# Kernel tuning notes

Hardware: AMD Instinct MI355X
Metric: run time of the kernel (lower is better)

## Reference

```python
import math
import jax, jax.numpy as jnp
import numpy as np

D = 768      # hidden_size
H = 16       # num_attention_heads (hardcoded in module)
DH = D // H  # value dim per head
SEQ = 512    # fpos/tpos are taken modulo 512
EPS = 1e-5   # torch LayerNorm default
SCALE = math.sqrt(D / H)  # attention_head_size = dim_key_query_all / num_heads


def _collab_attn(h, fpos, tpos, Wq, Wk, Wcb, Wv, bv, mix, Wd, bd, lng, lnb):
    """CollaborativeAttention.forward on one segment. h: [SEQ, D]."""
    fpos = fpos % SEQ
    tpos = tpos % SEQ
    fs = h[fpos]                                   # [F, D] gathered 'from' nodes
    ts = h[tpos]                                   # [T, D] gathered 'to' nodes
    q = fs @ Wq.T                                  # [F, D] (no bias)
    k = ts @ Wk.T                                  # [T, D] (no bias)
    mq = q[None, :, :] * mix[:, None, :]           # [H, F, D] per-head mixing
    scores = jnp.einsum('hfd,td->hft', mq, k)      # [H, F, T] full-D contraction
    cb = (ts @ Wcb.T).T                            # [H, T] content bias
    scores = (scores + cb[:, None, :]) / SCALE
    probs = jax.nn.softmax(scores, axis=-1)        # dropout = identity at eval
    v = (ts @ Wv.T + bv).reshape(-1, H, DH).transpose(1, 0, 2)  # [H, T, DH]
    ctx = jnp.einsum('hft,htd->hfd', probs, v)     # [H, F, DH]
    ctx = ctx.transpose(1, 0, 2).reshape(-1, D) @ Wd.T + bd      # [F, D]
    x = fs + ctx                                   # residual on gathered nodes
    mu = x.mean(-1, keepdims=True)
    var = ((x - mu) ** 2).mean(-1, keepdims=True)
    return lng * (x - mu) / jnp.sqrt(var + EPS) + lnb


def _encoder(hidden_states, fpos, tpos, qtoc, ctoq):
    outs = []
    for b in range(3):  # fixed small segment count, matches original unrolling
        o1 = _collab_attn(hidden_states[b], fpos[b], tpos[b], *qtoc).mean(0)
        o2 = _collab_attn(hidden_states[b], tpos[b], fpos[b], *ctoq).mean(0)
        outs.append(jnp.concatenate([o1, o2]))
    return jnp.stack(outs)  # [3, 2*D]


def setup_inputs() -> dict:
    key = jax.random.key(0)
    ks = jax.random.split(key, 32)
    inp = {
        'hidden_states': jax.random.normal(ks[0], (3, SEQ, D), jnp.float32),
        'fpos': jax.random.randint(ks[1], (3, 2048), 0, SEQ, jnp.int32),
        'tpos': jax.random.randint(ks[2], (3, 2048), 0, SEQ, jnp.int32),
    }
    i = 3
    for p in ('qtoc', 'ctoq'):
        for n, shape, std in (('Wq', (D, D), 0.02), ('Wk', (D, D), 0.02),
                              ('Wcb', (H, D), 0.02), ('Wv', (D, D), 0.02),
                              ('Wd', (D, D), 0.02), ('mix', (H, D), 0.2)):
            inp[p + '_' + n] = std * jax.random.normal(ks[i], shape, jnp.float32)
            i += 1
        inp[p + '_bv'] = jnp.zeros((D,), jnp.float32)
        inp[p + '_bd'] = jnp.zeros((D,), jnp.float32)
        inp[p + '_lng'] = jnp.ones((D,), jnp.float32)
        inp[p + '_lnb'] = jnp.zeros((D,), jnp.float32)
    return inp


def reference(hidden_states, fpos, tpos,
              qtoc_Wq, qtoc_Wk, qtoc_Wcb, qtoc_Wv, qtoc_Wd, qtoc_mix,
              qtoc_bv, qtoc_bd, qtoc_lng, qtoc_lnb,
              ctoq_Wq, ctoq_Wk, ctoq_Wcb, ctoq_Wv, ctoq_Wd, ctoq_mix,
              ctoq_bv, ctoq_bd, ctoq_lng, ctoq_lnb):
    qtoc = (qtoc_Wq, qtoc_Wk, qtoc_Wcb, qtoc_Wv, qtoc_bv, qtoc_mix,
            qtoc_Wd, qtoc_bd, qtoc_lng, qtoc_lnb)
    ctoq = (ctoq_Wq, ctoq_Wk, ctoq_Wcb, ctoq_Wv, ctoq_bv, ctoq_mix,
            ctoq_Wd, ctoq_bd, ctoq_lng, ctoq_lnb)
    return _encoder(hidden_states, fpos, tpos, qtoc, ctoq)
```

## Files before the change

kernel.cpp:

```cpp
#include <hip/hip_runtime.h>
#include <math.h>

#define DD 768
#define HH 16
#define DHH 48
#define NPOS 512
#define NIDX 2048
#define INV_SCALE 0.14433756729740643f
#define LN_EPS 1e-5f

typedef __bf16 bf16_t;
typedef __bf16 bf16x8 __attribute__((ext_vector_type(8)));
typedef float f32x4 __attribute__((ext_vector_type(4)));

__device__ __forceinline__ void g2lds16(const void* g, void* l) {
  __builtin_amdgcn_global_load_lds((const __attribute__((address_space(1))) void*)g,
                                   (__attribute__((address_space(3))) void*)l, 16, 0, 0);
}

struct CvtDesc { const float* src; bf16_t* dst; int n8; };
struct CvtBatch { CvtDesc d[9]; };

__global__ __launch_bounds__(256) void prep(const int* __restrict__ fpos,
                                            const int* __restrict__ tpos,
                                            int* __restrict__ CNT, CvtBatch cvb,
                                            const float* __restrict__ hs,
                                            const float* __restrict__ Wcb0,
                                            const float* __restrict__ Wcb1,
                                            float* __restrict__ cbG) {
  const int bid = blockIdx.x;
  const int tid = threadIdx.x;
  __shared__ int shist[NPOS];
  if (bid < 6) {
    const int b = bid >> 1, which = bid & 1;
    const int* src = (which ? tpos : fpos) + b * NIDX;
    for (int i = tid; i < NPOS; i += 256) shist[i] = 0;
    __syncthreads();
    for (int i = tid; i < NIDX; i += 256) atomicAdd(&shist[src[i] & (NPOS - 1)], 1);
    __syncthreads();
    for (int i = tid; i < NPOS; i += 256) CNT[bid * NPOS + i] = shist[i];
  } else if (bid < 582) {
    const CvtDesc de = cvb.d[(bid - 6) >> 6];
    for (int i = ((bid - 6) & 63) * 256 + tid; i < de.n8; i += 64 * 256) {
      const f32x4 a = *(const f32x4*)(de.src + (size_t)i * 8);
      const f32x4 b = *(const f32x4*)(de.src + (size_t)i * 8 + 4);
      bf16_t t[8];
#pragma unroll
      for (int e = 0; e < 4; ++e) { t[e] = (bf16_t)a[e]; t[4 + e] = (bf16_t)b[e]; }
      *(bf16x8*)(de.dst + (size_t)i * 8) = *(bf16x8*)t;
    }
  } else {
    const int g = bid - 582;
    const int pd = g >> 5, t0 = (g & 31) * 16;
    const int b = pd >> 1;
    const float* W = (pd & 1) ? Wcb1 : Wcb0;
    const int tl = tid >> 4, hh = tid & 15;
    const float* hrow = hs + ((size_t)b * NPOS + t0 + tl) * DD;
    const float* wrow = W + hh * DD;
    float s = 0.f;
    for (int k = 0; k < DD; k += 4) {
      const f32x4 a = *(const f32x4*)(hrow + k);
      const f32x4 bq = *(const f32x4*)(wrow + k);
      s += a[0] * bq[0] + a[1] * bq[1] + a[2] * bq[2] + a[3] * bq[3];
    }
    cbG[((size_t)pd * NPOS + t0 + tl) * HH + hh] = s;
  }
}

struct MDesc { const bf16_t* A; const bf16_t* B; const float* bias; void* C; int mode; };
struct MBatch { MDesc d[18]; };

__global__ __launch_bounds__(256, 4) void gemm64(MBatch batch) {
  const MDesc de = batch.d[blockIdx.y];
  const int mt = blockIdx.x & 7, nt = blockIdx.x >> 3;
  const int m0 = mt * 64, n0 = nt * 128;

  __shared__ bf16_t SA[2][2048];
  __shared__ bf16_t SB[2][4096];

  const int tid = threadIdx.x;
  const int w = tid >> 6, lane = tid & 63;
  const int wm = w >> 1, wn = w & 1;
  const int lm = lane & 15, lq = lane >> 4;
  const int sr = lane >> 2, sq = lane & 3;

  f32x4 acc[2][4] = {};

  auto stage = [&](int buf, int k0) {
#pragma unroll
    for (int c = 0; c < 3; ++c) {
      const int issue = w + c * 4;
      if (issue < 4)
        g2lds16(de.A + (size_t)(m0 + issue * 16 + sr) * 768 + k0 + sq * 8,
                SA[buf] + issue * 512);
      else {
        const int e = issue - 4;
        g2lds16(de.B + (size_t)(n0 + e * 16 + sr) * 768 + k0 + sq * 8,
                SB[buf] + e * 512);
      }
    }
  };

  stage(0, 0);
  for (int k0i = 0; k0i < 24; ++k0i) {
    const int cur = k0i & 1;
    __syncthreads();
    if (k0i + 1 < 24) stage(cur ^ 1, (k0i + 1) * 32);
    bf16x8 af[2], bfr[4];
#pragma unroll
    for (int i = 0; i < 2; ++i)
      af[i] = *(const bf16x8*)(SA[cur] + (wm * 32 + i * 16 + lm) * 32 + lq * 8);
#pragma unroll
    for (int j = 0; j < 4; ++j)
      bfr[j] = *(const bf16x8*)(SB[cur] + (wn * 64 + j * 16 + lm) * 32 + lq * 8);
#pragma unroll
    for (int i = 0; i < 2; ++i)
#pragma unroll
      for (int j = 0; j < 4; ++j)
        acc[i][j] = __builtin_amdgcn_mfma_f32_16x16x32_bf16(af[i], bfr[j], acc[i][j], 0, 0, 0);
  }

#pragma unroll
  for (int i = 0; i < 2; ++i) {
    const int rbase = m0 + wm * 32 + i * 16 + lq * 4;
#pragma unroll
    for (int j = 0; j < 4; ++j) {
      const int c = n0 + wn * 64 + j * 16 + lm;
      const float bv = de.bias ? de.bias[c] : 0.f;
#pragma unroll
      for (int r = 0; r < 4; ++r) {
        const float v = acc[i][j][r] + bv;
        if (de.mode == 0)      ((float*)de.C)[(size_t)(rbase + r) * 768 + c] = v;
        else if (de.mode == 1) ((bf16_t*)de.C)[(size_t)(rbase + r) * 768 + c] = (bf16_t)v;
        else                   ((bf16_t*)de.C)[(size_t)c * NPOS + rbase + r] = (bf16_t)v;
      }
    }
  }
}

__global__ __launch_bounds__(256, 4) void attn_mfma(
    const bf16_t* __restrict__ Qg, const bf16_t* __restrict__ Kg,
    const bf16_t* __restrict__ Vt, const float* __restrict__ cbG,
    const int* __restrict__ CNT, const float* __restrict__ mix0,
    const float* __restrict__ mix1, bf16_t* __restrict__ CTX) {
  const int bid = blockIdx.x;
  const int ft = bid & 7, h = (bid >> 3) & 15, pd = bid >> 7;
  const int dir = pd & 1;
  const int f0 = ft * 64;

  __shared__ bf16_t U[17408];
  __shared__ float mixs[768];
  __shared__ float cbw[512];
  __shared__ float rowl[64];

  const int tid = threadIdx.x;
  const int w = tid >> 6, lane = tid & 63;
  const bf16_t* Qp = Qg + (size_t)pd * NPOS * DD;
  const bf16_t* Kp = Kg + (size_t)pd * NPOS * DD;
  const bf16_t* Vp = Vt + (size_t)pd * DD * NPOS + (size_t)h * DHH * NPOS;
  const float* mix = (dir ? mix1 : mix0) + h * DD;
  const int* cnt = CNT + ((pd & ~1) + (1 - dir)) * NPOS;

  for (int i = tid; i < 768; i += 256) mixs[i] = mix[i] * INV_SCALE;
  for (int i = tid; i < 512; i += 256)
    cbw[i] = cbG[((size_t)pd * NPOS + i) * HH + h] * INV_SCALE + __logf((float)cnt[i]);

  const int wm = w >> 1, wn = w & 1;
  const int lm = lane & 15, lq = lane >> 4;
  const int sr = lane >> 2, sq = lane & 3;

  f32x4 pv[4] = {};

  for (int jt = 0; jt < 4; ++jt) {
    const int j0 = jt * 128;
    __syncthreads();

    auto stage = [&](int buf, int k0) {
#pragma unroll
      for (int c = 0; c < 3; ++c) {
        const int issue = w + c * 4;
        if (issue < 4)
          g2lds16(Qp + (size_t)(f0 + issue * 16 + sr) * DD + k0 + sq * 8,
                  U + buf * 6144 + issue * 512);
        else {
          const int e = issue - 4;
          g2lds16(Kp + (size_t)(j0 + e * 16 + sr) * DD + k0 + sq * 8,
                  U + buf * 6144 + 2048 + e * 512);
        }
      }
    };

    stage(0, 0);
    f32x4 sa[2][4] = {};
    for (int k0i = 0; k0i < 24; ++k0i) {
      const int cur = k0i & 1;
      const int k0 = k0i * 32;
      __syncthreads();
      if (k0i + 1 < 24) stage(cur ^ 1, k0 + 32);
      const f32x4 mxa = *(const f32x4*)&mixs[k0 + lq * 8];
      const f32x4 mxb = *(const f32x4*)&mixs[k0 + lq * 8 + 4];
      bf16x8 af[2], bfr[4];
#pragma unroll
      for (int i = 0; i < 2; ++i) {
        const bf16x8 q = *(const bf16x8*)(U + cur * 6144 + (wm * 32 + i * 16 + lm) * 32 + lq * 8);
        bf16_t t[8];
#pragma unroll
        for (int e = 0; e < 4; ++e) {
          t[e]     = (bf16_t)((float)q[e] * mxa[e]);
          t[4 + e] = (bf16_t)((float)q[4 + e] * mxb[e]);
        }
        af[i] = *(bf16x8*)t;
      }
#pragma unroll
      for (int j = 0; j < 4; ++j)
        bfr[j] = *(const bf16x8*)(U + cur * 6144 + 2048 + (wn * 64 + j * 16 + lm) * 32 + lq * 8);
#pragma unroll
      for (int i = 0; i < 2; ++i)
#pragma unroll
        for (int j = 0; j < 4; ++j)
          sa[i][j] = __builtin_amdgcn_mfma_f32_16x16x32_bf16(af[i], bfr[j], sa[i][j], 0, 0, 0);
    }
    __syncthreads();

#pragma unroll
    for (int j = 0; j < 4; ++j) {
      const int col = wn * 64 + j * 16 + lm;
      const float cb = cbw[j0 + col];
#pragma unroll
      for (int i = 0; i < 2; ++i) {
        const int rbase = wm * 32 + i * 16 + lq * 4;
#pragma unroll
        for (int r = 0; r < 4; ++r)
          U[(rbase + r) * 136 + col] = (bf16_t)__expf(sa[i][j][r] + cb);
      }
    }
    for (int i = tid; i < 49 * 16; i += 256) {
      const int r = i >> 4, cc = i & 15;
      if (r < 48)
        *(bf16x8*)(U + 8704 + r * 136 + cc * 8) =
            *(const bf16x8*)(Vp + (size_t)r * NPOS + j0 + cc * 8);
      else {
        bf16_t ones[8];
#pragma unroll
        for (int e = 0; e < 8; ++e) ones[e] = (bf16_t)1.f;
        *(bf16x8*)(U + 8704 + 48 * 136 + cc * 8) = *(bf16x8*)ones;
      }
    }
    __syncthreads();

#pragma unroll
    for (int kk = 0; kk < 4; ++kk) {
      const bf16x8 pa = *(const bf16x8*)(U + (w * 16 + lm) * 136 + kk * 32 + lq * 8);
#pragma unroll
      for (int j = 0; j < 4; ++j) {
        const bf16x8 pb = *(const bf16x8*)(U + 8704 + (j * 16 + lm) * 136 + kk * 32 + lq * 8);
        pv[j] = __builtin_amdgcn_mfma_f32_16x16x32_bf16(pa, pb, pv[j], 0, 0, 0);
      }
    }
  }

  if (lm == 0) {
#pragma unroll
    for (int r = 0; r < 4; ++r) rowl[w * 16 + lq * 4 + r] = pv[3][r];
  }
  __syncthreads();
#pragma unroll
  for (int j = 0; j < 3; ++j) {
#pragma unroll
    for (int r = 0; r < 4; ++r) {
      const int fr = w * 16 + lq * 4 + r;
      CTX[((size_t)pd * NPOS + f0 + fr) * DD + h * DHH + j * 16 + lm] =
          (bf16_t)(pv[j][r] / rowl[fr]);
    }
  }
}

__global__ __launch_bounds__(256) void ln_mean_kernel(
    const float* __restrict__ hs, const float* __restrict__ XB,
    const int* __restrict__ CNT,
    const float* __restrict__ lng0, const float* __restrict__ lnb0,
    const float* __restrict__ lng1, const float* __restrict__ lnb1,
    float* __restrict__ out) {
  const int blk = blockIdx.x;
  const int chunk = blk & 15;
  const int pd = blk >> 4;
  const int b = pd >> 1, dir = pd & 1;
  const float* lng = dir ? lng1 : lng0;
  const float* lnb = dir ? lnb1 : lnb0;
  const int* cnt = CNT + pd * NPOS;
  const float* hb = hs + (size_t)b * NPOS * DD;
  const float* xb = XB + (size_t)pd * NPOS * DD;

  __shared__ float wacc[4][DD];
  const int tid = threadIdx.x;
  const int wave = tid >> 6, lane = tid & 63;
  for (int d0 = tid; d0 < 4 * DD; d0 += 256) ((float*)wacc)[d0] = 0.f;
  __syncthreads();

  float lg[12], lb[12];
#pragma unroll
  for (int qd = 0; qd < 12; ++qd) {
    lg[qd] = lng[lane + qd * 64];
    lb[qd] = lnb[lane + qd * 64];
  }

  for (int rr = 0; rr < 8; ++rr) {
    const int p = chunk * 32 + wave * 8 + rr;
    float x[12];
    float s = 0.f, ss = 0.f;
#pragma unroll
    for (int qd = 0; qd < 12; ++qd) {
      const int d0 = lane + qd * 64;
      const float xv = hb[(size_t)p * DD + d0] + xb[(size_t)p * DD + d0];
      x[qd] = xv; s += xv; ss += xv * xv;
    }
#pragma unroll
    for (int o = 1; o < 64; o <<= 1) {
      s += __shfl_xor(s, o);
      ss += __shfl_xor(ss, o);
    }
    const float mu = s * (1.f / 768.f);
    const float var = ss * (1.f / 768.f) - mu * mu;
    const float rstd = rsqrtf(var + LN_EPS);
    const float wgt = (float)cnt[p];
    if (wgt != 0.f) {
#pragma unroll
      for (int qd = 0; qd < 12; ++qd) {
        const int d0 = lane + qd * 64;
        wacc[wave][d0] += wgt * (lg[qd] * (x[qd] - mu) * rstd + lb[qd]);
      }
    }
  }
  __syncthreads();
  for (int d0 = tid; d0 < DD; d0 += 256) {
    const float t = wacc[0][d0] + wacc[1][d0] + wacc[2][d0] + wacc[3][d0];
    atomicAdd(&out[b * 1536 + dir * 768 + d0], t * (1.f / 2048.f));
  }
}

extern "C" void kernel_launch(void* const* d_in, const int* in_sizes, int n_in,
                              void* d_out, int out_size, void* d_ws, size_t ws_size,
                              hipStream_t stream) {
  const float* hs  = (const float*)d_in[0];
  const int* fpos  = (const int*)d_in[1];
  const int* tpos  = (const int*)d_in[2];

  const float* Wq[2]; const float* Wk[2]; const float* Wcb[2]; const float* Wv[2];
  const float* Wd[2]; const float* mixp[2];
  const float* bv[2]; const float* bd[2]; const float* lng[2]; const float* lnb[2];
  for (int p = 0; p < 2; ++p) {
    const int base = 3 + p * 10;
    Wq[p]   = (const float*)d_in[base + 0];
    Wk[p]   = (const float*)d_in[base + 1];
    Wcb[p]  = (const float*)d_in[base + 2];
    Wv[p]   = (const float*)d_in[base + 3];
    Wd[p]   = (const float*)d_in[base + 4];
    mixp[p] = (const float*)d_in[base + 5];
    bv[p]   = (const float*)d_in[base + 6];
    bd[p]   = (const float*)d_in[base + 7];
    lng[p]  = (const float*)d_in[base + 8];
    lnb[p]  = (const float*)d_in[base + 9];
  }

  char* wsp = (char*)d_ws;
  size_t off = 0;
  auto alloc = [&](size_t bytes) { char* p = wsp + off; off = (off + bytes + 255) & ~(size_t)255; return p; };
  bf16_t* hsb  = (bf16_t*)alloc((size_t)3 * NPOS * DD * 2);
  bf16_t* Wb   = (bf16_t*)alloc((size_t)8 * DD * DD * 2);
  bf16_t* Qbf  = (bf16_t*)alloc((size_t)6 * NPOS * DD * 2);
  bf16_t* Kbf  = (bf16_t*)alloc((size_t)6 * NPOS * DD * 2);
  bf16_t* VtG  = (bf16_t*)alloc((size_t)6 * DD * NPOS * 2);
  bf16_t* CTXb = (bf16_t*)alloc((size_t)6 * NPOS * DD * 2);
  float*  XB   = (float*) alloc((size_t)6 * NPOS * DD * 4);
  float*  cbG  = (float*) alloc((size_t)6 * NPOS * HH * 4);
  int*    CNTb = (int*)   alloc((size_t)6 * NPOS * 4);

  hipMemsetAsync(d_out, 0, (size_t)out_size * sizeof(float), stream);

  CvtBatch cvb{};
  cvb.d[0] = CvtDesc{hs, hsb, 3 * NPOS * DD / 8};
  const float* wsrc[8] = {Wq[0], Wk[0], Wv[0], Wd[0], Wq[1], Wk[1], Wv[1], Wd[1]};
  for (int i = 0; i < 8; ++i)
    cvb.d[1 + i] = CvtDesc{wsrc[i], Wb + (size_t)i * DD * DD, DD * DD / 8};
  prep<<<774, 256, 0, stream>>>(fpos, tpos, CNTb, cvb, hs, Wcb[0], Wcb[1], cbG);

  MBatch gb{};
  int n = 0;
  for (int b = 0; b < 3; ++b)
    for (int p = 0; p < 2; ++p) {
      const int pd = b * 2 + p;
      const bf16_t* A = hsb + (size_t)b * NPOS * DD;
      const size_t o = (size_t)pd * NPOS * DD;
      gb.d[n++] = MDesc{A, Wb + (size_t)(p * 4 + 0) * DD * DD, nullptr, Qbf + o, 1};
      gb.d[n++] = MDesc{A, Wb + (size_t)(p * 4 + 1) * DD * DD, nullptr, Kbf + o, 1};
      gb.d[n++] = MDesc{A, Wb + (size_t)(p * 4 + 2) * DD * DD, bv[p],   VtG + (size_t)pd * DD * NPOS, 2};
    }
  gemm64<<<dim3(48, 18), 256, 0, stream>>>(gb);

  attn_mfma<<<768, 256, 0, stream>>>(Qbf, Kbf, VtG, cbG, CNTb, mixp[0], mixp[1], CTXb);

  MBatch gd{};
  for (int b = 0; b < 3; ++b)
    for (int p = 0; p < 2; ++p) {
      const int pd = b * 2 + p;
      const size_t o = (size_t)pd * NPOS * DD;
      gd.d[pd] = MDesc{CTXb + o, Wb + (size_t)(p * 4 + 3) * DD * DD, bd[p], XB + o, 0};
    }
  gemm64<<<dim3(48, 6), 256, 0, stream>>>(gd);

  ln_mean_kernel<<<96, 256, 0, stream>>>(hs, XB, CNTb, lng[0], lnb[0], lng[1], lnb[1],
                                         (float*)d_out);
}
```

Measured before the change: 288.2 us.

## Fuse content-bias into K GEMM, swizzle LDS, pre-mix Q per head, widen LN grid

The content-bias projection is folded into the K projection GEMM by appending the Wcb rows, zero-padded, to Wk, so the separate dot-product blocks in prep go away. LDS staging and reads gain an XOR swizzle to cut bank conflicts in both the GEMM and attention kernels. When workspace allows, a new qmix kernel writes a per-head mixed and scaled Q tensor, so the attention inner loop skips the per-element multiply, at the cost of a large extra memory write and read. The LayerNorm-mean kernel uses four times as many blocks with fewer rows each, and attention launch bounds drop to 3 blocks per CU.

```diff
diff --git a/kernel.cpp b/kernel.cpp
--- a/kernel.cpp
+++ b/kernel.cpp
@@ -17,17 +17,17 @@
   __builtin_amdgcn_global_load_lds((const __attribute__((address_space(1))) void*)g,
                                    (__attribute__((address_space(3))) void*)l, 16, 0, 0);
 }
+__device__ __forceinline__ int stg_chunk(int lane) { return (lane & 3) ^ ((lane >> 3) & 3); }
+__device__ __forceinline__ int rd_off(int row, int lq) {
+  return row * 32 + ((lq ^ ((row >> 1) & 3)) << 3);
+}
 
 struct CvtDesc { const float* src; bf16_t* dst; int n8; };
-struct CvtBatch { CvtDesc d[9]; };
+struct CvtBatch { CvtDesc d[13]; };
 
 __global__ __launch_bounds__(256) void prep(const int* __restrict__ fpos,
                                             const int* __restrict__ tpos,
-                                            int* __restrict__ CNT, CvtBatch cvb,
-                                            const float* __restrict__ hs,
-                                            const float* __restrict__ Wcb0,
-                                            const float* __restrict__ Wcb1,
-                                            float* __restrict__ cbG) {
+                                            int* __restrict__ CNT, CvtBatch cvb) {
   const int bid = blockIdx.x;
   const int tid = threadIdx.x;
   __shared__ int shist[NPOS];
@@ -39,40 +39,54 @@
     for (int i = tid; i < NIDX; i += 256) atomicAdd(&shist[src[i] & (NPOS - 1)], 1);
     __syncthreads();
     for (int i = tid; i < NPOS; i += 256) CNT[bid * NPOS + i] = shist[i];
-  } else if (bid < 582) {
-    const CvtDesc de = cvb.d[(bid - 6) >> 6];
-    for (int i = ((bid - 6) & 63) * 256 + tid; i < de.n8; i += 64 * 256) {
+    return;
+  }
+  const CvtDesc de = cvb.d[(bid - 6) >> 6];
+  for (int i = ((bid - 6) & 63) * 256 + tid; i < de.n8; i += 64 * 256) {
+    bf16_t t[8];
+    if (de.src) {
       const f32x4 a = *(const f32x4*)(de.src + (size_t)i * 8);
       const f32x4 b = *(const f32x4*)(de.src + (size_t)i * 8 + 4);
-      bf16_t t[8];
 #pragma unroll
       for (int e = 0; e < 4; ++e) { t[e] = (bf16_t)a[e]; t[4 + e] = (bf16_t)b[e]; }
-      *(bf16x8*)(de.dst + (size_t)i * 8) = *(bf16x8*)t;
-    }
-  } else {
-    const int g = bid - 582;
-    const int pd = g >> 5, t0 = (g & 31) * 16;
-    const int b = pd >> 1;
-    const float* W = (pd & 1) ? Wcb1 : Wcb0;
-    const int tl = tid >> 4, hh = tid & 15;
-    const float* hrow = hs + ((size_t)b * NPOS + t0 + tl) * DD;
-    const float* wrow = W + hh * DD;
-    float s = 0.f;
-    for (int k = 0; k < DD; k += 4) {
-      const f32x4 a = *(const f32x4*)(hrow + k);
-      const f32x4 bq = *(const f32x4*)(wrow + k);
-      s += a[0] * bq[0] + a[1] * bq[1] + a[2] * bq[2] + a[3] * bq[3];
-    }
-    cbG[((size_t)pd * NPOS + t0 + tl) * HH + hh] = s;
-  }
-}
-
-struct MDesc { const bf16_t* A; const bf16_t* B; const float* bias; void* C; int mode; };
+    } else {
+#pragma unroll
+      for (int e = 0; e < 8; ++e) t[e] = (bf16_t)0.f;
+    }
+    *(bf16x8*)(de.dst + (size_t)i * 8) = *(bf16x8*)t;
+  }
+}
+
+__global__ __launch_bounds__(256) void qmix(const bf16_t* __restrict__ Qbf,
+                                            const float* __restrict__ mix0,
+                                            const float* __restrict__ mix1,
+                                            bf16_t* __restrict__ Qm) {
+  const int idx = blockIdx.x * 256 + threadIdx.x;
+  const int c = idx % 96;
+  const int f = (idx / 96) & 511;
+  const int h = (idx / (96 * 512)) & 15;
+  const int pd = idx / (96 * 512 * 16);
+  const bf16x8 q = *(const bf16x8*)(Qbf + ((size_t)pd * NPOS + f) * DD + c * 8);
+  const float* m = ((pd & 1) ? mix1 : mix0) + h * DD + c * 8;
+  const f32x4 m0 = *(const f32x4*)m;
+  const f32x4 m1 = *(const f32x4*)(m + 4);
+  bf16_t t[8];
+#pragma unroll
+  for (int e = 0; e < 4; ++e) {
+    t[e]     = (bf16_t)((float)q[e] * m0[e] * INV_SCALE);
+    t[4 + e] = (bf16_t)((float)q[4 + e] * m1[e] * INV_SCALE);
+  }
+  *(bf16x8*)(Qm + ((size_t)(pd * 16 + h) * NPOS + f) * DD + c * 8) = *(bf16x8*)t;
+}
+
+struct MDesc { const bf16_t* A; const bf16_t* B; const float* bias; void* C;
+               float* cb; int mode; int ntiles; };
 struct MBatch { MDesc d[18]; };
 
 __global__ __launch_bounds__(256, 4) void gemm64(MBatch batch) {
   const MDesc de = batch.d[blockIdx.y];
   const int mt = blockIdx.x & 7, nt = blockIdx.x >> 3;
+  if (nt >= de.ntiles) return;
   const int m0 = mt * 64, n0 = nt * 128;
 
   __shared__ bf16_t SA[2][2048];
@@ -82,7 +96,7 @@
   const int w = tid >> 6, lane = tid & 63;
   const int wm = w >> 1, wn = w & 1;
   const int lm = lane & 15, lq = lane >> 4;
-  const int sr = lane >> 2, sq = lane & 3;
+  const int sr = lane >> 2, sc = stg_chunk(lane);
 
   f32x4 acc[2][4] = {};
 
@@ -91,11 +105,11 @@
     for (int c = 0; c < 3; ++c) {
       const int issue = w + c * 4;
       if (issue < 4)
-        g2lds16(de.A + (size_t)(m0 + issue * 16 + sr) * 768 + k0 + sq * 8,
+        g2lds16(de.A + (size_t)(m0 + issue * 16 + sr) * 768 + k0 + sc * 8,
                 SA[buf] + issue * 512);
       else {
         const int e = issue - 4;
-        g2lds16(de.B + (size_t)(n0 + e * 16 + sr) * 768 + k0 + sq * 8,
+        g2lds16(de.B + (size_t)(n0 + e * 16 + sr) * 768 + k0 + sc * 8,
                 SB[buf] + e * 512);
       }
     }
@@ -109,10 +123,10 @@
     bf16x8 af[2], bfr[4];
 #pragma unroll
     for (int i = 0; i < 2; ++i)
-      af[i] = *(const bf16x8*)(SA[cur] + (wm * 32 + i * 16 + lm) * 32 + lq * 8);
+      af[i] = *(const bf16x8*)(SA[cur] + rd_off(wm * 32 + i * 16 + lm, lq));
 #pragma unroll
     for (int j = 0; j < 4; ++j)
-      bfr[j] = *(const bf16x8*)(SB[cur] + (wn * 64 + j * 16 + lm) * 32 + lq * 8);
+      bfr[j] = *(const bf16x8*)(SB[cur] + rd_off(wn * 64 + j * 16 + lm, lq));
 #pragma unroll
     for (int i = 0; i < 2; ++i)
 #pragma unroll
@@ -126,48 +140,57 @@
 #pragma unroll
     for (int j = 0; j < 4; ++j) {
       const int c = n0 + wn * 64 + j * 16 + lm;
-      const float bv = de.bias ? de.bias[c] : 0.f;
+      const float bv = (de.bias && c < 768) ? de.bias[c] : 0.f;
 #pragma unroll
       for (int r = 0; r < 4; ++r) {
         const float v = acc[i][j][r] + bv;
         if (de.mode == 0)      ((float*)de.C)[(size_t)(rbase + r) * 768 + c] = v;
         else if (de.mode == 1) ((bf16_t*)de.C)[(size_t)(rbase + r) * 768 + c] = (bf16_t)v;
-        else                   ((bf16_t*)de.C)[(size_t)c * NPOS + rbase + r] = (bf16_t)v;
-      }
-    }
-  }
-}
-
-__global__ __launch_bounds__(256, 4) void attn_mfma(
-    const bf16_t* __restrict__ Qg, const bf16_t* __restrict__ Kg,
-    const bf16_t* __restrict__ Vt, const float* __restrict__ cbG,
-    const int* __restrict__ CNT, const float* __restrict__ mix0,
-    const float* __restrict__ mix1, bf16_t* __restrict__ CTX) {
+        else if (de.mode == 2) ((bf16_t*)de.C)[(size_t)c * NPOS + rbase + r] = (bf16_t)v;
+        else {
+          if (c < 768)       ((bf16_t*)de.C)[(size_t)(rbase + r) * 768 + c] = (bf16_t)v;
+          else if (c < 784)  de.cb[(size_t)(rbase + r) * 16 + (c - 768)] = v;
+        }
+      }
+    }
+  }
+}
+
+template <int PRE>
+__global__ __launch_bounds__(256, 3) void attn_mfma(
+    const bf16_t* __restrict__ Qg, const bf16_t* __restrict__ Qm,
+    const bf16_t* __restrict__ Kg, const bf16_t* __restrict__ Vt,
+    const float* __restrict__ cbG, const int* __restrict__ CNT,
+    const float* __restrict__ mix0, const float* __restrict__ mix1,
+    bf16_t* __restrict__ CTX) {
   const int bid = blockIdx.x;
   const int ft = bid & 7, h = (bid >> 3) & 15, pd = bid >> 7;
   const int dir = pd & 1;
   const int f0 = ft * 64;
 
   __shared__ bf16_t U[17408];
-  __shared__ float mixs[768];
+  __shared__ float mixs[PRE ? 4 : 768];
   __shared__ float cbw[512];
   __shared__ float rowl[64];
 
   const int tid = threadIdx.x;
   const int w = tid >> 6, lane = tid & 63;
-  const bf16_t* Qp = Qg + (size_t)pd * NPOS * DD;
+  const bf16_t* Qp = PRE ? (Qm + (size_t)(pd * 16 + h) * NPOS * DD)
+                         : (Qg + (size_t)pd * NPOS * DD);
   const bf16_t* Kp = Kg + (size_t)pd * NPOS * DD;
   const bf16_t* Vp = Vt + (size_t)pd * DD * NPOS + (size_t)h * DHH * NPOS;
-  const float* mix = (dir ? mix1 : mix0) + h * DD;
   const int* cnt = CNT + ((pd & ~1) + (1 - dir)) * NPOS;
 
-  for (int i = tid; i < 768; i += 256) mixs[i] = mix[i] * INV_SCALE;
+  if (!PRE) {
+    const float* mix = (dir ? mix1 : mix0) + h * DD;
+    for (int i = tid; i < 768; i += 256) mixs[i] = mix[i] * INV_SCALE;
+  }
   for (int i = tid; i < 512; i += 256)
     cbw[i] = cbG[((size_t)pd * NPOS + i) * HH + h] * INV_SCALE + __logf((float)cnt[i]);
 
   const int wm = w >> 1, wn = w & 1;
   const int lm = lane & 15, lq = lane >> 4;
-  const int sr = lane >> 2, sq = lane & 3;
+  const int sr = lane >> 2, sc = stg_chunk(lane);
 
   f32x4 pv[4] = {};
 
@@ -180,11 +203,11 @@
       for (int c = 0; c < 3; ++c) {
         const int issue = w + c * 4;
         if (issue < 4)
-          g2lds16(Qp + (size_t)(f0 + issue * 16 + sr) * DD + k0 + sq * 8,
+          g2lds16(Qp + (size_t)(f0 + issue * 16 + sr) * DD + k0 + sc * 8,
                   U + buf * 6144 + issue * 512);
         else {
           const int e = issue - 4;
-          g2lds16(Kp + (size_t)(j0 + e * 16 + sr) * DD + k0 + sq * 8,
+          g2lds16(Kp + (size_t)(j0 + e * 16 + sr) * DD + k0 + sc * 8,
                   U + buf * 6144 + 2048 + e * 512);
         }
       }
@@ -197,23 +220,28 @@
       const int k0 = k0i * 32;
       __syncthreads();
       if (k0i + 1 < 24) stage(cur ^ 1, k0 + 32);
-      const f32x4 mxa = *(const f32x4*)&mixs[k0 + lq * 8];
-      const f32x4 mxb = *(const f32x4*)&mixs[k0 + lq * 8 + 4];
       bf16x8 af[2], bfr[4];
 #pragma unroll
       for (int i = 0; i < 2; ++i) {
-        const bf16x8 q = *(const bf16x8*)(U + cur * 6144 + (wm * 32 + i * 16 + lm) * 32 + lq * 8);
-        bf16_t t[8];
-#pragma unroll
-        for (int e = 0; e < 4; ++e) {
-          t[e]     = (bf16_t)((float)q[e] * mxa[e]);
-          t[4 + e] = (bf16_t)((float)q[4 + e] * mxb[e]);
+        const int off = cur * 6144 + rd_off(wm * 32 + i * 16 + lm, lq);
+        if (PRE) {
+          af[i] = *(const bf16x8*)(U + off);
+        } else {
+          const f32x4 mxa = *(const f32x4*)&mixs[k0 + lq * 8];
+          const f32x4 mxb = *(const f32x4*)&mixs[k0 + lq * 8 + 4];
+          const bf16x8 q = *(const bf16x8*)(U + off);
+          bf16_t t[8];
+#pragma unroll
+          for (int e = 0; e < 4; ++e) {
+            t[e]     = (bf16_t)((float)q[e] * mxa[e]);
+            t[4 + e] = (bf16_t)((float)q[4 + e] * mxb[e]);
+          }
+          af[i] = *(bf16x8*)t;
         }
-        af[i] = *(bf16x8*)t;
       }
 #pragma unroll
       for (int j = 0; j < 4; ++j)
-        bfr[j] = *(const bf16x8*)(U + cur * 6144 + 2048 + (wn * 64 + j * 16 + lm) * 32 + lq * 8);
+        bfr[j] = *(const bf16x8*)(U + cur * 6144 + 2048 + rd_off(wn * 64 + j * 16 + lm, lq));
 #pragma unroll
       for (int i = 0; i < 2; ++i)
 #pragma unroll
@@ -282,8 +310,8 @@
     const float* __restrict__ lng1, const float* __restrict__ lnb1,
     float* __restrict__ out) {
   const int blk = blockIdx.x;
-  const int chunk = blk & 15;
-  const int pd = blk >> 4;
+  const int chunk = blk & 63;
+  const int pd = blk >> 6;
   const int b = pd >> 1, dir = pd & 1;
   const float* lng = dir ? lng1 : lng0;
   const float* lnb = dir ? lnb1 : lnb0;
@@ -304,8 +332,8 @@
     lb[qd] = lnb[lane + qd * 64];
   }
 
-  for (int rr = 0; rr < 8; ++rr) {
-    const int p = chunk * 32 + wave * 8 + rr;
+  for (int rr = 0; rr < 2; ++rr) {
+    const int p = chunk * 8 + wave * 2 + rr;
     float x[12];
     float s = 0.f, ss = 0.f;
 #pragma unroll
@@ -366,7 +394,8 @@
   size_t off = 0;
   auto alloc = [&](size_t bytes) { char* p = wsp + off; off = (off + bytes + 255) & ~(size_t)255; return p; };
   bf16_t* hsb  = (bf16_t*)alloc((size_t)3 * NPOS * DD * 2);
-  bf16_t* Wb   = (bf16_t*)alloc((size_t)8 * DD * DD * 2);
+  bf16_t* Wb   = (bf16_t*)alloc((size_t)6 * DD * DD * 2);
+  bf16_t* WkCb = (bf16_t*)alloc((size_t)2 * 896 * DD * 2);
   bf16_t* Qbf  = (bf16_t*)alloc((size_t)6 * NPOS * DD * 2);
   bf16_t* Kbf  = (bf16_t*)alloc((size_t)6 * NPOS * DD * 2);
   bf16_t* VtG  = (bf16_t*)alloc((size_t)6 * DD * NPOS * 2);
@@ -374,15 +403,24 @@
   float*  XB   = (float*) alloc((size_t)6 * NPOS * DD * 4);
   float*  cbG  = (float*) alloc((size_t)6 * NPOS * HH * 4);
   int*    CNTb = (int*)   alloc((size_t)6 * NPOS * 4);
+  const size_t qm_bytes = (size_t)6 * HH * NPOS * DD * 2;
+  const int use_pre = (off + qm_bytes + 4096 <= ws_size);
+  bf16_t* Qm = use_pre ? (bf16_t*)alloc(qm_bytes) : nullptr;
 
   hipMemsetAsync(d_out, 0, (size_t)out_size * sizeof(float), stream);
 
   CvtBatch cvb{};
   cvb.d[0] = CvtDesc{hs, hsb, 3 * NPOS * DD / 8};
-  const float* wsrc[8] = {Wq[0], Wk[0], Wv[0], Wd[0], Wq[1], Wk[1], Wv[1], Wd[1]};
-  for (int i = 0; i < 8; ++i)
-    cvb.d[1 + i] = CvtDesc{wsrc[i], Wb + (size_t)i * DD * DD, DD * DD / 8};
-  prep<<<774, 256, 0, stream>>>(fpos, tpos, CNTb, cvb, hs, Wcb[0], Wcb[1], cbG);
+  for (int p = 0; p < 2; ++p) {
+    cvb.d[1 + p * 3] = CvtDesc{Wq[p], Wb + (size_t)(p * 3 + 0) * DD * DD, DD * DD / 8};
+    cvb.d[2 + p * 3] = CvtDesc{Wv[p], Wb + (size_t)(p * 3 + 1) * DD * DD, DD * DD / 8};
+    cvb.d[3 + p * 3] = CvtDesc{Wd[p], Wb + (size_t)(p * 3 + 2) * DD * DD, DD * DD / 8};
+    bf16_t* wk = WkCb + (size_t)p * 896 * DD;
+    cvb.d[7 + p * 3] = CvtDesc{Wk[p], wk, DD * DD / 8};
+    cvb.d[8 + p * 3] = CvtDesc{Wcb[p], wk + (size_t)768 * DD, 16 * DD / 8};
+    cvb.d[9 + p * 3] = CvtDesc{nullptr, wk + (size_t)784 * DD, 112 * DD / 8};
+  }
+  prep<<<838, 256, 0, stream>>>(fpos, tpos, CNTb, cvb);
 
   MBatch gb{};
   int n = 0;
@@ -391,23 +429,33 @@
       const int pd = b * 2 + p;
       const bf16_t* A = hsb + (size_t)b * NPOS * DD;
       const size_t o = (size_t)pd * NPOS * DD;
-      gb.d[n++] = MDesc{A, Wb + (size_t)(p * 4 + 0) * DD * DD, nullptr, Qbf + o, 1};
-      gb.d[n++] = MDesc{A, Wb + (size_t)(p * 4 + 1) * DD * DD, nullptr, Kbf + o, 1};
-      gb.d[n++] = MDesc{A, Wb + (size_t)(p * 4 + 2) * DD * DD, bv[p],   VtG + (size_t)pd * DD * NPOS, 2};
-    }
-  gemm64<<<dim3(48, 18), 256, 0, stream>>>(gb);
-
-  attn_mfma<<<768, 256, 0, stream>>>(Qbf, Kbf, VtG, cbG, CNTb, mixp[0], mixp[1], CTXb);
+      gb.d[n++] = MDesc{A, Wb + (size_t)(p * 3 + 0) * DD * DD, nullptr, Qbf + o, nullptr, 1, 6};
+      gb.d[n++] = MDesc{A, WkCb + (size_t)p * 896 * DD, nullptr, Kbf + o,
+                        cbG + (size_t)pd * NPOS * HH, 3, 7};
+      gb.d[n++] = MDesc{A, Wb + (size_t)(p * 3 + 1) * DD * DD, bv[p],
+                        VtG + (size_t)pd * DD * NPOS, nullptr, 2, 6};
+    }
+  gemm64<<<dim3(56, 18), 256, 0, stream>>>(gb);
+
+  if (use_pre) {
+    qmix<<<18432, 256, 0, stream>>>(Qbf, mixp[0], mixp[1], Qm);
+    attn_mfma<1><<<768, 256, 0, stream>>>(Qbf, Qm, Kbf, VtG, cbG, CNTb,
+                                          mixp[0], mixp[1], CTXb);
+  } else {
+    attn_mfma<0><<<768, 256, 0, stream>>>(Qbf, Qbf, Kbf, VtG, cbG, CNTb,
+                                          mixp[0], mixp[1], CTXb);
+  }
 
   MBatch gd{};
   for (int b = 0; b < 3; ++b)
     for (int p = 0; p < 2; ++p) {
       const int pd = b * 2 + p;
       const size_t o = (size_t)pd * NPOS * DD;
-      gd.d[pd] = MDesc{CTXb + o, Wb + (size_t)(p * 4 + 3) * DD * DD, bd[p], XB + o, 0};
-    }
-  gemm64<<<dim3(48, 6), 256, 0, stream>>>(gd);
-
-  ln_mean_kernel<<<96, 256, 0, stream>>>(hs, XB, CNTb, lng[0], lnb[0], lng[1], lnb[1],
-                                         (float*)d_out);
-}
+      gd.d[pd] = MDesc{CTXb + o, Wb + (size_t)(p * 3 + 2) * DD * DD, bd[p],
+                       XB + o, nullptr, 0, 6};
+    }
+  gemm64<<<dim3(56, 6), 256, 0, stream>>>(gd);
+
+  ln_mean_kernel<<<384, 256, 0, stream>>>(hs, XB, CNTb, lng[0], lnb[0], lng[1], lnb[1],
+                                          (float*)d_out);
+}
```

New measurement: 260.3 us. 9.7% less time.
